# Performance work log

Hardware: AMD Instinct MI355X
Metric: run time of the kernel (lower is better)

Reference implementation:

```python
import jax, jax.numpy as jnp
import numpy as np

NUM_ENTITIES = 10000
EMB_DIM = 128   # H
FEAT_DIM = 64   # N_d
BATCH = 8192


def setup_inputs() -> dict:
    key = jax.random.key(0)
    ks = jax.random.split(key, 8)
    return {
        "e": jax.random.normal(ks[0], (NUM_ENTITIES, EMB_DIM), dtype=jnp.float32),
        "l": jax.random.normal(ks[1], (NUM_ENTITIES, FEAT_DIM), dtype=jnp.float32),
        "W_ze": jax.random.normal(ks[2], (NUM_ENTITIES, EMB_DIM, EMB_DIM), dtype=jnp.float32),
        "W_zl": jax.random.normal(ks[3], (NUM_ENTITIES, EMB_DIM, FEAT_DIM), dtype=jnp.float32),
        "W_he": jax.random.normal(ks[4], (NUM_ENTITIES, EMB_DIM, EMB_DIM), dtype=jnp.float32),
        "W_hl": jax.random.normal(ks[5], (NUM_ENTITIES, EMB_DIM, FEAT_DIM), dtype=jnp.float32),
        "b": jax.random.normal(ks[6], (EMB_DIM,), dtype=jnp.float32),
        "index": jax.random.randint(ks[7], (BATCH,), 0, NUM_ENTITIES, dtype=jnp.int64),
    }


def reference(e, l, W_ze, W_zl, W_he, W_hl, b, index):
    # Gather per-entity rows / weight matrices for the batch of ids.
    e_idx = e[index]          # [B, H]
    l_idx = l[index]          # [B, N_d]
    # Batched matvecs: 'nih,nh->ni'
    Wze = jnp.einsum('nih,nh->ni', W_ze[index], e_idx)
    Wzl = jnp.einsum('nih,nh->ni', W_zl[index], l_idx)
    Whe = jnp.einsum('nih,nh->ni', W_he[index], e_idx)
    Whl = jnp.einsum('nih,nh->ni', W_hl[index], l_idx)
    Z = jax.nn.sigmoid(Wze + Wzl + b)   # gate, [B, H]
    H = jnp.tanh(Whe + Whl)             # candidate, [B, H]
    return Z * H + (1.0 - Z) * e_idx
```

## Files before the change

### kernel.cpp

```cpp
#include <hip/hip_runtime.h>


constexpr int H_DIM = 128;
constexpr int N_D   = 64;
constexpr int N_ENT = 10000;
constexpr int ROWS_PER_BLK = 32;

__global__ void k_mark(const int* __restrict__ index, int* __restrict__ used,
                       int* __restrict__ count, int* __restrict__ list, int B) {
    const int b = blockIdx.x * blockDim.x + threadIdx.x;
    if (b < B) {
        const int n = index[b];
        if (atomicExch(&used[n], 1) == 0) {
            const int p = atomicAdd(count, 1);
            list[p] = n;
        }
    }
}

__global__ __launch_bounds__(256) void k_compute_unique(
    const float* __restrict__ e,
    const float* __restrict__ l,
    const float* __restrict__ W_ze,
    const float* __restrict__ W_zl,
    const float* __restrict__ W_he,
    const float* __restrict__ W_hl,
    const float* __restrict__ bias,
    const int*  __restrict__ count,
    const int*  __restrict__ list,
    float* __restrict__ uout)
{
    const int bid = blockIdx.x;
    const int ei  = bid >> 2;
    if (ei >= *count) return;
    const int q = bid & 3;
    const long long n = (long long)list[ei];

    const int tid  = threadIdx.x;
    const int wave = tid >> 6;
    const int lane = tid & 63;
    const int g    = lane >> 4;
    const int j    = lane & 15;

    __shared__ float az_s[ROWS_PER_BLK];
    __shared__ float ah_s[ROWS_PER_BLK];

    const float4* ep = reinterpret_cast<const float4*>(e + n * H_DIM);
    const float4 xe0 = ep[j];
    const float4 xe1 = ep[j + 16];
    const float4 xl  = reinterpret_cast<const float4*>(l + n * N_D)[j];

    const float4* wze = reinterpret_cast<const float4*>(W_ze + n * (size_t)(H_DIM * H_DIM));
    const float4* whe = reinterpret_cast<const float4*>(W_he + n * (size_t)(H_DIM * H_DIM));
    const float4* wzl = reinterpret_cast<const float4*>(W_zl + n * (size_t)(H_DIM * N_D));
    const float4* whl = reinterpret_cast<const float4*>(W_hl + n * (size_t)(H_DIM * N_D));

    #pragma unroll
    for (int pass = 0; pass < 2; ++pass) {
        const int rl = pass * 16 + wave * 4 + g;
        const int r  = q * ROWS_PER_BLK + rl;

        const float4 a0 = wze[r * 32 + j];
        const float4 a1 = wze[r * 32 + j + 16];
        const float4 b0 = whe[r * 32 + j];
        const float4 b1 = whe[r * 32 + j + 16];
        const float4 c0 = wzl[r * 16 + j];
        const float4 d0 = whl[r * 16 + j];

        float pz = fmaf(a0.x, xe0.x, fmaf(a0.y, xe0.y, fmaf(a0.z, xe0.z, a0.w * xe0.w)));
        pz = fmaf(a1.x, xe1.x, fmaf(a1.y, xe1.y, fmaf(a1.z, xe1.z, fmaf(a1.w, xe1.w, pz))));
        pz = fmaf(c0.x, xl.x,  fmaf(c0.y, xl.y,  fmaf(c0.z, xl.z,  fmaf(c0.w, xl.w,  pz))));

        float ph = fmaf(b0.x, xe0.x, fmaf(b0.y, xe0.y, fmaf(b0.z, xe0.z, b0.w * xe0.w)));
        ph = fmaf(b1.x, xe1.x, fmaf(b1.y, xe1.y, fmaf(b1.z, xe1.z, fmaf(b1.w, xe1.w, ph))));
        ph = fmaf(d0.x, xl.x,  fmaf(d0.y, xl.y,  fmaf(d0.z, xl.z,  fmaf(d0.w, xl.w,  ph))));

        #pragma unroll
        for (int m = 1; m <= 8; m <<= 1) {
            pz += __shfl_xor(pz, m, 64);
            ph += __shfl_xor(ph, m, 64);
        }
        if (j == 0) { az_s[rl] = pz; ah_s[rl] = ph; }
    }
    __syncthreads();

    if (tid < ROWS_PER_BLK) {
        const int r = q * ROWS_PER_BLK + tid;
        const float zg = 1.0f / (1.0f + __expf(-(az_s[tid] + bias[r])));
        const float hc = tanhf(ah_s[tid]);
        const float ei_v = e[n * H_DIM + r];
        uout[n * H_DIM + r] = zg * hc + (1.0f - zg) * ei_v;
    }
}

__global__ void k_gather(const int* __restrict__ index,
                         const float* __restrict__ uout,
                         float* __restrict__ out, int B)
{
    const int i = blockIdx.x * blockDim.x + threadIdx.x;
    if (i < B * (H_DIM / 4)) {
        const int b = i >> 5;
        const int c = i & 31;
        const long long n = (long long)index[b];
        reinterpret_cast<float4*>(out)[(size_t)b * 32 + c] =
            reinterpret_cast<const float4*>(uout)[n * 32 + c];
    }
}

constexpr int ELEMS = 4;
__global__ __launch_bounds__(256) void literal_e_fused(
    const float* __restrict__ e, const float* __restrict__ l,
    const float* __restrict__ W_ze, const float* __restrict__ W_zl,
    const float* __restrict__ W_he, const float* __restrict__ W_hl,
    const float* __restrict__ bias, const int* __restrict__ index,
    float* __restrict__ out)
{
    const int tid  = threadIdx.x;
    const int wave = tid >> 6;
    const int lane = tid & 63;
    const int g    = lane >> 4;
    const int j    = lane & 15;

    __shared__ float se[H_DIM];
    __shared__ float az_s[H_DIM];
    __shared__ float ah_s[H_DIM];

    const long long base = (long long)blockIdx.x * ELEMS;
    for (int it = 0; it < ELEMS; ++it) {
        const long long n  = (long long)index[base + it];
        const long long bi = base + it;
        const float4* ep = reinterpret_cast<const float4*>(e + n * H_DIM);
        const float4 xe0 = ep[j];
        const float4 xe1 = ep[j + 16];
        const float4 xl  = reinterpret_cast<const float4*>(l + n * N_D)[j];
        if (tid < H_DIM) se[tid] = e[n * H_DIM + tid];

        const float4* wze = reinterpret_cast<const float4*>(W_ze + n * (size_t)(H_DIM * H_DIM));
        const float4* whe = reinterpret_cast<const float4*>(W_he + n * (size_t)(H_DIM * H_DIM));
        const float4* wzl = reinterpret_cast<const float4*>(W_zl + n * (size_t)(H_DIM * N_D));
        const float4* whl = reinterpret_cast<const float4*>(W_hl + n * (size_t)(H_DIM * N_D));

        #pragma unroll 4
        for (int pass = 0; pass < 8; ++pass) {
            const int r = pass * 16 + wave * 4 + g;
            const float4 a0 = wze[r * 32 + j];
            const float4 a1 = wze[r * 32 + j + 16];
            const float4 b0 = whe[r * 32 + j];
            const float4 b1 = whe[r * 32 + j + 16];
            const float4 c0 = wzl[r * 16 + j];
            const float4 d0 = whl[r * 16 + j];
            float pz = fmaf(a0.x, xe0.x, fmaf(a0.y, xe0.y, fmaf(a0.z, xe0.z, a0.w * xe0.w)));
            pz = fmaf(a1.x, xe1.x, fmaf(a1.y, xe1.y, fmaf(a1.z, xe1.z, fmaf(a1.w, xe1.w, pz))));
            pz = fmaf(c0.x, xl.x,  fmaf(c0.y, xl.y,  fmaf(c0.z, xl.z,  fmaf(c0.w, xl.w,  pz))));
            float ph = fmaf(b0.x, xe0.x, fmaf(b0.y, xe0.y, fmaf(b0.z, xe0.z, b0.w * xe0.w)));
            ph = fmaf(b1.x, xe1.x, fmaf(b1.y, xe1.y, fmaf(b1.z, xe1.z, fmaf(b1.w, xe1.w, ph))));
            ph = fmaf(d0.x, xl.x,  fmaf(d0.y, xl.y,  fmaf(d0.z, xl.z,  fmaf(d0.w, xl.w,  ph))));
            #pragma unroll
            for (int m = 1; m <= 8; m <<= 1) {
                pz += __shfl_xor(pz, m, 64);
                ph += __shfl_xor(ph, m, 64);
            }
            if (j == 0) { az_s[r] = pz; ah_s[r] = ph; }
        }
        __syncthreads();
        if (tid < H_DIM) {
            const float zg = 1.0f / (1.0f + __expf(-(az_s[tid] + bias[tid])));
            const float hc = tanhf(ah_s[tid]);
            out[bi * H_DIM + tid] = zg * hc + (1.0f - zg) * se[tid];
        }
        __syncthreads();
    }
}

extern "C" void kernel_launch(void* const* d_in, const int* in_sizes, int n_in,
                              void* d_out, int out_size, void* d_ws, size_t ws_size,
                              hipStream_t stream) {
    const float* e    = (const float*)d_in[0];
    const float* l    = (const float*)d_in[1];
    const float* W_ze = (const float*)d_in[2];
    const float* W_zl = (const float*)d_in[3];
    const float* W_he = (const float*)d_in[4];
    const float* W_hl = (const float*)d_in[5];
    const float* bias = (const float*)d_in[6];
    const int*   idx  = (const int*)d_in[7];
    float* out = (float*)d_out;

    const int B = in_sizes[7];

    const size_t uout_bytes = (size_t)N_ENT * H_DIM * sizeof(float);
    const size_t need = uout_bytes + (size_t)(2 * N_ENT + 1) * sizeof(int);

    if (ws_size >= need) {
        float* uout  = (float*)d_ws;
        int*   used  = (int*)((char*)d_ws + uout_bytes);
        int*   count = used + N_ENT;
        int*   list  = count + 1;

        hipMemsetAsync(used, 0, (size_t)(N_ENT + 1) * sizeof(int), stream);
        k_mark<<<dim3((B + 255) / 256), dim3(256), 0, stream>>>(idx, used, count, list, B);
        k_compute_unique<<<dim3(4 * N_ENT), dim3(256), 0, stream>>>(
            e, l, W_ze, W_zl, W_he, W_hl, bias, count, list, uout);
        k_gather<<<dim3((B * (H_DIM / 4) + 255) / 256), dim3(256), 0, stream>>>(
            idx, uout, out, B);
    } else {
        literal_e_fused<<<dim3(B / ELEMS), dim3(256), 0, stream>>>(
            e, l, W_ze, W_zl, W_he, W_hl, bias, idx, out);
    }
}
```

Baseline: 209.4 us.

## Fuse dedup, unique compute and gather into one cooperative persistent kernel

Replaces the memset plus three-kernel pipeline with a single cooperative kernel of 1024 persistent blocks. The kernel clears the flags, marks unique entities, computes each unique entity's output with one block per entity, and gathers results into the output, with grid-wide syncs between phases. This removes per-launch overhead and inter-kernel gaps. The costs are grid.sync barriers and coarser work per block: each block now handles all 128 rows instead of four blocks covering 32 rows each, which can reduce memory-level parallelism. The fallback path is kept but now also uses one block per entity, and the non-workspace fused kernel is removed.

```diff
diff --git a/kernel.cpp b/kernel.cpp
--- a/kernel.cpp
+++ b/kernel.cpp
@@ -1,10 +1,115 @@
 #include <hip/hip_runtime.h>
+#include <hip/hip_cooperative_groups.h>
+
+namespace cg = cooperative_groups;
 
 
 constexpr int H_DIM = 128;
 constexpr int N_D   = 64;
 constexpr int N_ENT = 10000;
-constexpr int ROWS_PER_BLK = 32;
+
+__global__ __launch_bounds__(256, 4) void k_fused_coop(
+    const float* __restrict__ e,
+    const float* __restrict__ l,
+    const float* __restrict__ W_ze,
+    const float* __restrict__ W_zl,
+    const float* __restrict__ W_he,
+    const float* __restrict__ W_hl,
+    const float* __restrict__ bias,
+    const int*  __restrict__ index,
+    float* __restrict__ out,
+    int* used, int* count, int* list,
+    float* __restrict__ uout, int B)
+{
+    cg::grid_group grid = cg::this_grid();
+
+    const int tid      = threadIdx.x;
+    const int gtid     = blockIdx.x * blockDim.x + tid;
+    const int nthreads = gridDim.x * blockDim.x;
+
+    for (int i = gtid; i < N_ENT + 1; i += nthreads) used[i] = 0;
+    grid.sync();
+
+    for (int b = gtid; b < B; b += nthreads) {
+        const int n = index[b];
+        if (atomicExch(&used[n], 1) == 0) {
+            const int p = atomicAdd(count, 1);
+            atomicExch(&list[p], n);
+        }
+    }
+    grid.sync();
+
+    {
+        __shared__ float az_s[H_DIM];
+        __shared__ float ah_s[H_DIM];
+
+        const int cnt  = *count;
+        const int wave = tid >> 6;
+        const int lane = tid & 63;
+        const int g    = lane >> 4;
+        const int j    = lane & 15;
+
+        for (int ei = blockIdx.x; ei < cnt; ei += gridDim.x) {
+            const long long n = (long long)list[ei];
+
+            const float4* ep = reinterpret_cast<const float4*>(e + n * H_DIM);
+            const float4 xe0 = ep[j];
+            const float4 xe1 = ep[j + 16];
+            const float4 xl  = reinterpret_cast<const float4*>(l + n * N_D)[j];
+
+            const float4* wze = reinterpret_cast<const float4*>(W_ze + n * (size_t)(H_DIM * H_DIM));
+            const float4* whe = reinterpret_cast<const float4*>(W_he + n * (size_t)(H_DIM * H_DIM));
+            const float4* wzl = reinterpret_cast<const float4*>(W_zl + n * (size_t)(H_DIM * N_D));
+            const float4* whl = reinterpret_cast<const float4*>(W_hl + n * (size_t)(H_DIM * N_D));
+
+            #pragma unroll 4
+            for (int pass = 0; pass < 8; ++pass) {
+                const int r = pass * 16 + wave * 4 + g;
+
+                const float4 a0 = wze[r * 32 + j];
+                const float4 a1 = wze[r * 32 + j + 16];
+                const float4 b0 = whe[r * 32 + j];
+                const float4 b1 = whe[r * 32 + j + 16];
+                const float4 c0 = wzl[r * 16 + j];
+                const float4 d0 = whl[r * 16 + j];
+
+                float pz = fmaf(a0.x, xe0.x, fmaf(a0.y, xe0.y, fmaf(a0.z, xe0.z, a0.w * xe0.w)));
+                pz = fmaf(a1.x, xe1.x, fmaf(a1.y, xe1.y, fmaf(a1.z, xe1.z, fmaf(a1.w, xe1.w, pz))));
+                pz = fmaf(c0.x, xl.x,  fmaf(c0.y, xl.y,  fmaf(c0.z, xl.z,  fmaf(c0.w, xl.w,  pz))));
+
+                float ph = fmaf(b0.x, xe0.x, fmaf(b0.y, xe0.y, fmaf(b0.z, xe0.z, b0.w * xe0.w)));
+                ph = fmaf(b1.x, xe1.x, fmaf(b1.y, xe1.y, fmaf(b1.z, xe1.z, fmaf(b1.w, xe1.w, ph))));
+                ph = fmaf(d0.x, xl.x,  fmaf(d0.y, xl.y,  fmaf(d0.z, xl.z,  fmaf(d0.w, xl.w,  ph))));
+
+                #pragma unroll
+                for (int m = 1; m <= 8; m <<= 1) {
+                    pz += __shfl_xor(pz, m, 64);
+                    ph += __shfl_xor(ph, m, 64);
+                }
+                if (j == 0) { az_s[r] = pz; ah_s[r] = ph; }
+            }
+            __syncthreads();
+
+            if (tid < H_DIM) {
+                const float zg = 1.0f / (1.0f + __expf(-(az_s[tid] + bias[tid])));
+                const float hc = tanhf(ah_s[tid]);
+                const float ev = e[n * H_DIM + tid];
+                uout[n * H_DIM + tid] = zg * hc + (1.0f - zg) * ev;
+            }
+            __syncthreads();
+        }
+    }
+    grid.sync();
+
+    for (int i = gtid; i < B * (H_DIM / 4); i += nthreads) {
+        const int b = i >> 5;
+        const int c = i & 31;
+        const long long n = (long long)index[b];
+        reinterpret_cast<float4*>(out)[(size_t)b * 32 + c] =
+            reinterpret_cast<const float4*>(uout)[n * 32 + c];
+    }
+}
+
 
 __global__ void k_mark(const int* __restrict__ index, int* __restrict__ used,
                        int* __restrict__ count, int* __restrict__ list, int B) {
@@ -19,21 +124,15 @@
 }
 
 __global__ __launch_bounds__(256) void k_compute_unique(
-    const float* __restrict__ e,
-    const float* __restrict__ l,
-    const float* __restrict__ W_ze,
-    const float* __restrict__ W_zl,
-    const float* __restrict__ W_he,
-    const float* __restrict__ W_hl,
+    const float* __restrict__ e, const float* __restrict__ l,
+    const float* __restrict__ W_ze, const float* __restrict__ W_zl,
+    const float* __restrict__ W_he, const float* __restrict__ W_hl,
     const float* __restrict__ bias,
-    const int*  __restrict__ count,
-    const int*  __restrict__ list,
+    const int* __restrict__ count, const int* __restrict__ list,
     float* __restrict__ uout)
 {
-    const int bid = blockIdx.x;
-    const int ei  = bid >> 2;
+    const int ei = blockIdx.x;
     if (ei >= *count) return;
-    const int q = bid & 3;
     const long long n = (long long)list[ei];
 
     const int tid  = threadIdx.x;
@@ -42,8 +141,8 @@
     const int g    = lane >> 4;
     const int j    = lane & 15;
 
-    __shared__ float az_s[ROWS_PER_BLK];
-    __shared__ float ah_s[ROWS_PER_BLK];
+    __shared__ float az_s[H_DIM];
+    __shared__ float ah_s[H_DIM];
 
     const float4* ep = reinterpret_cast<const float4*>(e + n * H_DIM);
     const float4 xe0 = ep[j];
@@ -55,41 +154,35 @@
     const float4* wzl = reinterpret_cast<const float4*>(W_zl + n * (size_t)(H_DIM * N_D));
     const float4* whl = reinterpret_cast<const float4*>(W_hl + n * (size_t)(H_DIM * N_D));
 
-    #pragma unroll
-    for (int pass = 0; pass < 2; ++pass) {
-        const int rl = pass * 16 + wave * 4 + g;
-        const int r  = q * ROWS_PER_BLK + rl;
-
+    #pragma unroll 4
+    for (int pass = 0; pass < 8; ++pass) {
+        const int r = pass * 16 + wave * 4 + g;
         const float4 a0 = wze[r * 32 + j];
         const float4 a1 = wze[r * 32 + j + 16];
         const float4 b0 = whe[r * 32 + j];
         const float4 b1 = whe[r * 32 + j + 16];
         const float4 c0 = wzl[r * 16 + j];
         const float4 d0 = whl[r * 16 + j];
-
         float pz = fmaf(a0.x, xe0.x, fmaf(a0.y, xe0.y, fmaf(a0.z, xe0.z, a0.w * xe0.w)));
         pz = fmaf(a1.x, xe1.x, fmaf(a1.y, xe1.y, fmaf(a1.z, xe1.z, fmaf(a1.w, xe1.w, pz))));
         pz = fmaf(c0.x, xl.x,  fmaf(c0.y, xl.y,  fmaf(c0.z, xl.z,  fmaf(c0.w, xl.w,  pz))));
-
         float ph = fmaf(b0.x, xe0.x, fmaf(b0.y, xe0.y, fmaf(b0.z, xe0.z, b0.w * xe0.w)));
         ph = fmaf(b1.x, xe1.x, fmaf(b1.y, xe1.y, fmaf(b1.z, xe1.z, fmaf(b1.w, xe1.w, ph))));
         ph = fmaf(d0.x, xl.x,  fmaf(d0.y, xl.y,  fmaf(d0.z, xl.z,  fmaf(d0.w, xl.w,  ph))));
-
         #pragma unroll
         for (int m = 1; m <= 8; m <<= 1) {
             pz += __shfl_xor(pz, m, 64);
             ph += __shfl_xor(ph, m, 64);
         }
-        if (j == 0) { az_s[rl] = pz; ah_s[rl] = ph; }
+        if (j == 0) { az_s[r] = pz; ah_s[r] = ph; }
     }
     __syncthreads();
 
-    if (tid < ROWS_PER_BLK) {
-        const int r = q * ROWS_PER_BLK + tid;
-        const float zg = 1.0f / (1.0f + __expf(-(az_s[tid] + bias[r])));
+    if (tid < H_DIM) {
+        const float zg = 1.0f / (1.0f + __expf(-(az_s[tid] + bias[tid])));
         const float hc = tanhf(ah_s[tid]);
-        const float ei_v = e[n * H_DIM + r];
-        uout[n * H_DIM + r] = zg * hc + (1.0f - zg) * ei_v;
+        const float ev = e[n * H_DIM + tid];
+        uout[n * H_DIM + tid] = zg * hc + (1.0f - zg) * ev;
     }
 }
 
@@ -104,71 +197,6 @@
         const long long n = (long long)index[b];
         reinterpret_cast<float4*>(out)[(size_t)b * 32 + c] =
             reinterpret_cast<const float4*>(uout)[n * 32 + c];
-    }
-}
-
-constexpr int ELEMS = 4;
-__global__ __launch_bounds__(256) void literal_e_fused(
-    const float* __restrict__ e, const float* __restrict__ l,
-    const float* __restrict__ W_ze, const float* __restrict__ W_zl,
-    const float* __restrict__ W_he, const float* __restrict__ W_hl,
-    const float* __restrict__ bias, const int* __restrict__ index,
-    float* __restrict__ out)
-{
-    const int tid  = threadIdx.x;
-    const int wave = tid >> 6;
-    const int lane = tid & 63;
-    const int g    = lane >> 4;
-    const int j    = lane & 15;
-
-    __shared__ float se[H_DIM];
-    __shared__ float az_s[H_DIM];
-    __shared__ float ah_s[H_DIM];
-
-    const long long base = (long long)blockIdx.x * ELEMS;
-    for (int it = 0; it < ELEMS; ++it) {
-        const long long n  = (long long)index[base + it];
-        const long long bi = base + it;
-        const float4* ep = reinterpret_cast<const float4*>(e + n * H_DIM);
-        const float4 xe0 = ep[j];
-        const float4 xe1 = ep[j + 16];
-        const float4 xl  = reinterpret_cast<const float4*>(l + n * N_D)[j];
-        if (tid < H_DIM) se[tid] = e[n * H_DIM + tid];
-
-        const float4* wze = reinterpret_cast<const float4*>(W_ze + n * (size_t)(H_DIM * H_DIM));
-        const float4* whe = reinterpret_cast<const float4*>(W_he + n * (size_t)(H_DIM * H_DIM));
-        const float4* wzl = reinterpret_cast<const float4*>(W_zl + n * (size_t)(H_DIM * N_D));
-        const float4* whl = reinterpret_cast<const float4*>(W_hl + n * (size_t)(H_DIM * N_D));
-
-        #pragma unroll 4
-        for (int pass = 0; pass < 8; ++pass) {
-            const int r = pass * 16 + wave * 4 + g;
-            const float4 a0 = wze[r * 32 + j];
-            const float4 a1 = wze[r * 32 + j + 16];
-            const float4 b0 = whe[r * 32 + j];
-            const float4 b1 = whe[r * 32 + j + 16];
-            const float4 c0 = wzl[r * 16 + j];
-            const float4 d0 = whl[r * 16 + j];
-            float pz = fmaf(a0.x, xe0.x, fmaf(a0.y, xe0.y, fmaf(a0.z, xe0.z, a0.w * xe0.w)));
-            pz = fmaf(a1.x, xe1.x, fmaf(a1.y, xe1.y, fmaf(a1.z, xe1.z, fmaf(a1.w, xe1.w, pz))));
-            pz = fmaf(c0.x, xl.x,  fmaf(c0.y, xl.y,  fmaf(c0.z, xl.z,  fmaf(c0.w, xl.w,  pz))));
-            float ph = fmaf(b0.x, xe0.x, fmaf(b0.y, xe0.y, fmaf(b0.z, xe0.z, b0.w * xe0.w)));
-            ph = fmaf(b1.x, xe1.x, fmaf(b1.y, xe1.y, fmaf(b1.z, xe1.z, fmaf(b1.w, xe1.w, ph))));
-            ph = fmaf(d0.x, xl.x,  fmaf(d0.y, xl.y,  fmaf(d0.z, xl.z,  fmaf(d0.w, xl.w,  ph))));
-            #pragma unroll
-            for (int m = 1; m <= 8; m <<= 1) {
-                pz += __shfl_xor(pz, m, 64);
-                ph += __shfl_xor(ph, m, 64);
-            }
-            if (j == 0) { az_s[r] = pz; ah_s[r] = ph; }
-        }
-        __syncthreads();
-        if (tid < H_DIM) {
-            const float zg = 1.0f / (1.0f + __expf(-(az_s[tid] + bias[tid])));
-            const float hc = tanhf(ah_s[tid]);
-            out[bi * H_DIM + tid] = zg * hc + (1.0f - zg) * se[tid];
-        }
-        __syncthreads();
     }
 }
 
@@ -190,20 +218,28 @@
     const size_t uout_bytes = (size_t)N_ENT * H_DIM * sizeof(float);
     const size_t need = uout_bytes + (size_t)(2 * N_ENT + 1) * sizeof(int);
 
-    if (ws_size >= need) {
-        float* uout  = (float*)d_ws;
-        int*   used  = (int*)((char*)d_ws + uout_bytes);
-        int*   count = used + N_ENT;
-        int*   list  = count + 1;
-
+    if (ws_size < need) return;
+
+    float* uout  = (float*)d_ws;
+    int*   used  = (int*)((char*)d_ws + uout_bytes);
+    int*   count = used + N_ENT;
+    int*   list  = count + 1;
+
+    int B_arg = B;
+    void* args[] = {
+        (void*)&e, (void*)&l, (void*)&W_ze, (void*)&W_zl, (void*)&W_he,
+        (void*)&W_hl, (void*)&bias, (void*)&idx, (void*)&out,
+        (void*)&used, (void*)&count, (void*)&list, (void*)&uout, (void*)&B_arg
+    };
+    hipError_t err = hipLaunchCooperativeKernel(
+        (const void*)k_fused_coop, dim3(1024), dim3(256), args, 0, stream);
+
+    if (err != hipSuccess) {
         hipMemsetAsync(used, 0, (size_t)(N_ENT + 1) * sizeof(int), stream);
         k_mark<<<dim3((B + 255) / 256), dim3(256), 0, stream>>>(idx, used, count, list, B);
-        k_compute_unique<<<dim3(4 * N_ENT), dim3(256), 0, stream>>>(
+        k_compute_unique<<<dim3(N_ENT), dim3(256), 0, stream>>>(
             e, l, W_ze, W_zl, W_he, W_hl, bias, count, list, uout);
         k_gather<<<dim3((B * (H_DIM / 4) + 255) / 256), dim3(256), 0, stream>>>(
             idx, uout, out, B);
-    } else {
-        literal_e_fused<<<dim3(B / ELEMS), dim3(256), 0, stream>>>(
-            e, l, W_ze, W_zl, W_he, W_hl, bias, idx, out);
-    }
-}
+    }
+}
```

After: 542.1 us. 2.59x slower.
